# Kernel optimization log

Measured on AMD Instinct MI355X. Metric: run time of the kernel, lower is better.

Reference implementation:

```python
import jax, jax.numpy as jnp
import numpy as np

B, D = 1024, 256
Q = 65536
K = 200
CLASSES = 10
TEMP = 0.07
EPS = 1e-12  # F.normalize default eps


def _l2_normalize(v):
    n = jnp.linalg.norm(v, axis=-1, keepdims=True)
    return v / jnp.maximum(n, EPS)


def setup_inputs() -> dict:
    key = jax.random.key(0)
    k1, k2, k3 = jax.random.split(key, 3)
    x = jax.random.normal(k1, (B, D), dtype=jnp.float32)
    # memory bank init mimics uniform(-stdv, stdv) with stdv = 1/sqrt(D/3)
    stdv = 1.0 / np.sqrt(D / 3.0)
    memory = jax.random.uniform(k2, (Q, D), dtype=jnp.float32, minval=-stdv, maxval=stdv)
    memory_label = jax.random.randint(k3, (Q,), 0, CLASSES, dtype=jnp.int64)
    return {"x": x, "memory": memory, "memory_label": memory_label}


def reference(x, memory, memory_label):
    # dist: [B, Q] cosine-ish similarity (memory not re-normalized in forward)
    dist = _l2_normalize(x) @ memory.T
    # eps_ball = 1.1 > 1 -> kNN top-k branch is always taken
    sim_weight, sim_indices = jax.lax.top_k(dist, K)          # [B, K]
    sim_labels = memory_label[sim_indices]                     # [B, K]
    w = jax.nn.softmax(sim_weight / TEMP, axis=1)              # [B, K]
    one_hot = jax.nn.one_hot(sim_labels, CLASSES, dtype=w.dtype)  # [B, K, C]
    pred_scores = jnp.sum(one_hot * w[:, :, None], axis=1)     # [B, C]
    pred_scores = jnp.minimum(pred_scores + 1e-5, 1.0)
    return pred_scores
```

## Files before the change

### kernel.cpp

```cpp
#include <hip/hip_runtime.h>
#include <hip/hip_bf16.h>

#define B_ROWS 1024
#define D_DIM 256
#define Q_N 65536
#define K_TOP 200
#define N_CLASSES 10
#define INV_T 14.2857142857142857f
#define NCOLS_S 4096
#define ST_SAMP 48u
#define SCAP 4096

typedef unsigned int u32;
typedef unsigned short u16;
typedef unsigned long long u64;

using bf16x8 = __attribute__((ext_vector_type(8))) __bf16;
using f32x4  = __attribute__((ext_vector_type(4))) float;


__device__ __forceinline__ u32 fkey(float f) {
  u32 u = __float_as_uint(f);
  return (u >> 31) ? ~u : (u | 0x80000000u);
}
__device__ __forceinline__ float funkey(u32 u) {
  return __uint_as_float((u >> 31) ? (u & 0x7fffffffu) : ~u);
}
__device__ __forceinline__ u16 bf16_rn(float f) {
  u32 u = __float_as_uint(f);
  u32 r = (u + 0x7fffu + ((u >> 16) & 1u)) >> 16;
  return (u16)r;
}
__device__ __forceinline__ void split2(float f, u16& h, u16& l) {
  u16 hh = bf16_rn(f);
  float hf = __uint_as_float(((u32)hh) << 16);
  h = hh;
  l = bf16_rn(f - hf);
}

__device__ __forceinline__ void gl16(const void* g, void* l) {
  __builtin_amdgcn_global_load_lds((const __attribute__((address_space(1))) u32*)g,
                                   (__attribute__((address_space(3))) u32*)l, 16, 0, 0);
}

__global__ __launch_bounds__(256) void xnorm_k(const float* __restrict__ x,
                                               u16* __restrict__ xh, u16* __restrict__ xl) {
  int row = blockIdx.x, t = threadIdx.x;
  int lane = t & 63, w = t >> 6;
  float v = x[row * D_DIM + t];
  float s = v * v;
  for (int o = 32; o > 0; o >>= 1) s += __shfl_down(s, o);
  __shared__ float ws[4];
  if (lane == 0) ws[w] = s;
  __syncthreads();
  if (t == 0) ws[0] = ws[0] + ws[1] + ws[2] + ws[3];
  __syncthreads();
  float inv = 1.0f / fmaxf(sqrtf(ws[0]), 1e-12f);
  u16 h, l;
  split2(v * inv, h, l);
  xh[row * D_DIM + t] = h;
  xl[row * D_DIM + t] = l;
}

__global__ __launch_bounds__(256) void mdecomp_k(const float4* __restrict__ m,
                                                 ushort4* __restrict__ mh,
                                                 ushort4* __restrict__ ml, int n4) {
  int i = blockIdx.x * blockDim.x + threadIdx.x;
  int stride = gridDim.x * blockDim.x;
  for (; i < n4; i += stride) {
    float4 v = m[i];
    ushort4 h, l;
    split2(v.x, h.x, l.x);
    split2(v.y, h.y, l.y);
    split2(v.z, h.z, l.z);
    split2(v.w, h.w, l.w);
    mh[i] = h;
    ml[i] = l;
  }
}

__device__ __forceinline__ void gemm_tile(const u16* __restrict__ Ah, const u16* __restrict__ Al,
                                          const u16* __restrict__ Bh, const u16* __restrict__ Bl,
                                          int trow0, int col0, int tid, u16* sm, f32x4 (&acc)[4][4]) {
  u16* sAh = sm;
  u16* sAl = sm + 4096;
  u16* sBh = sm + 8192;
  u16* sBl = sm + 12288;
  int lane = tid & 63, wid = tid >> 6;
  int wr = wid >> 1, wc = wid & 1;

  int r_s = wid * 32 + (lane >> 2);
  int c_s = (((lane & 3) ^ ((lane >> 3) & 3)) << 3);
  int ar0 = trow0 + r_s, ar1 = ar0 + 16;
  int br0 = col0 + r_s, br1 = br0 + 16;

  int fr = lane & 15, fq = lane >> 4;
  int cswz = (fq ^ ((fr >> 1) & 3)) * 8;
  int a_off0 = (wr * 64 + fr) * 32 + cswz;
  int b_off0 = (wc * 64 + fr) * 32 + cswz;

  for (int kt = 0; kt < 8; ++kt) {
    int k0 = kt * 32;
    gl16(Ah + (size_t)ar0 * D_DIM + k0 + c_s, &sAh[wid * 1024]);
    gl16(Ah + (size_t)ar1 * D_DIM + k0 + c_s, &sAh[wid * 1024 + 512]);
    gl16(Al + (size_t)ar0 * D_DIM + k0 + c_s, &sAl[wid * 1024]);
    gl16(Al + (size_t)ar1 * D_DIM + k0 + c_s, &sAl[wid * 1024 + 512]);
    gl16(Bh + (size_t)br0 * D_DIM + k0 + c_s, &sBh[wid * 1024]);
    gl16(Bh + (size_t)br1 * D_DIM + k0 + c_s, &sBh[wid * 1024 + 512]);
    gl16(Bl + (size_t)br0 * D_DIM + k0 + c_s, &sBl[wid * 1024]);
    gl16(Bl + (size_t)br1 * D_DIM + k0 + c_s, &sBl[wid * 1024 + 512]);
    __syncthreads();

    bf16x8 ah[4], al[4], bh[4], bl[4];
#pragma unroll
    for (int m = 0; m < 4; ++m) {
      ah[m] = *(const bf16x8*)&sAh[a_off0 + m * 512];
      al[m] = *(const bf16x8*)&sAl[a_off0 + m * 512];
    }
#pragma unroll
    for (int n = 0; n < 4; ++n) {
      bh[n] = *(const bf16x8*)&sBh[b_off0 + n * 512];
      bl[n] = *(const bf16x8*)&sBl[b_off0 + n * 512];
    }
#pragma unroll
    for (int m = 0; m < 4; ++m)
#pragma unroll
      for (int n = 0; n < 4; ++n) {
        acc[m][n] = __builtin_amdgcn_mfma_f32_16x16x32_bf16(ah[m], bh[n], acc[m][n], 0, 0, 0);
        acc[m][n] = __builtin_amdgcn_mfma_f32_16x16x32_bf16(ah[m], bl[n], acc[m][n], 0, 0, 0);
        acc[m][n] = __builtin_amdgcn_mfma_f32_16x16x32_bf16(al[m], bh[n], acc[m][n], 0, 0, 0);
      }
    __syncthreads();
  }
}

__global__ __launch_bounds__(256) void gemm_s_k(const u16* __restrict__ Ah, const u16* __restrict__ Al,
                                                const u16* __restrict__ Bh, const u16* __restrict__ Bl,
                                                float* __restrict__ dist_s) {
  __shared__ u16 sm[16384];
  int tid = threadIdx.x;
  int trow0 = blockIdx.x << 7, col0 = blockIdx.y << 7;
  f32x4 acc[4][4] = {};
  gemm_tile(Ah, Al, Bh, Bl, trow0, col0, tid, sm, acc);
  int lane = tid & 63, wid = tid >> 6;
  int wr = wid >> 1, wc = wid & 1, fr = lane & 15, fq = lane >> 4;
#pragma unroll
  for (int m = 0; m < 4; ++m) {
    int rr = trow0 + wr * 64 + m * 16 + fq * 4;
#pragma unroll
    for (int n = 0; n < 4; ++n) {
      int cc = col0 + wc * 64 + n * 16 + fr;
#pragma unroll
      for (int r = 0; r < 4; ++r)
        dist_s[(size_t)(rr + r) * NCOLS_S + cc] = acc[m][n][r];
    }
  }
}

__global__ __launch_bounds__(256) void thr_k(const float* __restrict__ dist_s,
                                             u32* __restrict__ tkeyA, u32* __restrict__ cnt) {
  __shared__ u32 shist[1024];
  __shared__ u32 wtot[4];
  int row = blockIdx.x, tid = threadIdx.x, lane = tid & 63, w = tid >> 6;
  const float4* dp = (const float4*)(dist_s + (size_t)row * NCOLS_S);
  shist[tid] = 0; shist[tid + 256] = 0; shist[tid + 512] = 0; shist[tid + 768] = 0;
  __syncthreads();
#pragma unroll
  for (int j = 0; j < 4; ++j) {
    float4 v = dp[tid + (j << 8)];
    atomicAdd(&shist[fkey(v.x) >> 22], 1u);
    atomicAdd(&shist[fkey(v.y) >> 22], 1u);
    atomicAdd(&shist[fkey(v.z) >> 22], 1u);
    atomicAdd(&shist[fkey(v.w) >> 22], 1u);
  }
  __syncthreads();
  u32 cs = shist[tid * 4] + shist[tid * 4 + 1] + shist[tid * 4 + 2] + shist[tid * 4 + 3];
  u32 sfx = cs;
#pragma unroll
  for (int off = 1; off < 64; off <<= 1) {
    u32 t = __shfl_down(sfx, off);
    sfx += (lane + off < 64) ? t : 0u;
  }
  if (lane == 0) wtot[w] = sfx;
  __syncthreads();
  u32 woff = 0;
  for (int j = w + 1; j < 4; ++j) woff += wtot[j];
  u32 S = sfx + woff, Safter = S - cs;
  if (S >= ST_SAMP && Safter < ST_SAMP) {
    u32 cum = Safter;
    int bin = tid * 4;
    for (int b = tid * 4 + 3; b >= tid * 4; --b) {
      u32 hb = shist[b];
      if (cum + hb >= ST_SAMP) { bin = b; break; }
      cum += hb;
    }
    tkeyA[row] = ((u32)bin) << 22;
  }
  if (tid == 0) cnt[row] = 0;
}

__global__ __launch_bounds__(256) void gemm_f_k(const u16* __restrict__ Ah, const u16* __restrict__ Al,
                                                const u16* __restrict__ Bh, const u16* __restrict__ Bl,
                                                const u32* __restrict__ tkeyA, u32* __restrict__ cnt,
                                                u64* __restrict__ cand, int cap) {
  __shared__ u16 sm[16384];
  __shared__ u32 sT[128];
  __shared__ u32 rcnt[128], rbase[128], rcur[128];
  __shared__ u32 scnt;
  int tid = threadIdx.x;
  int bid = blockIdx.x;
  int swz = (bid & 7) * 512 + (bid >> 3);
  int trow0 = (swz & 7) << 7;
  int col0 = (swz >> 3) << 7;
  if (tid < 128) { sT[tid] = tkeyA[trow0 + tid]; rcnt[tid] = 0; }
  if (tid == 0) scnt = 0;
  f32x4 acc[4][4] = {};
  gemm_tile(Ah, Al, Bh, Bl, trow0, col0, tid, sm, acc);

  u64* sbuf = (u64*)sm;
  int lane = tid & 63, wid = tid >> 6;
  int wr = wid >> 1, wc = wid & 1, fr = lane & 15, fq = lane >> 4;
#pragma unroll
  for (int m = 0; m < 4; ++m) {
    int lr0 = wr * 64 + m * 16 + fq * 4;
#pragma unroll
    for (int n = 0; n < 4; ++n) {
      int cc = col0 + wc * 64 + n * 16 + fr;
#pragma unroll
      for (int r = 0; r < 4; ++r) {
        u32 k = fkey(acc[m][n][r]);
        int lrow = lr0 + r;
        if (k >= sT[lrow]) {
          u32 s = atomicAdd(&scnt, 1u);
          if (s < (u32)SCAP) {
            sbuf[s] = ((u64)k << 32) | ((u64)(u32)lrow << 16) | (u64)(u32)cc;
            atomicAdd(&rcnt[lrow], 1u);
          } else {
            int grow = trow0 + lrow;
            u32 s2 = atomicAdd(&cnt[grow], 1u);
            if (s2 < (u32)cap) cand[(size_t)grow * cap + s2] = ((u64)k << 32) | (u32)(~(u32)cc);
          }
        }
      }
    }
  }
  __syncthreads();
  if (tid < 128) {
    u32 nr = rcnt[tid];
    rbase[tid] = nr ? atomicAdd(&cnt[trow0 + tid], nr) : 0u;
    rcur[tid] = 0;
  }
  __syncthreads();
  u32 total = min(scnt, (u32)SCAP);
  for (u32 i = tid; i < total; i += 256) {
    u64 e = sbuf[i];
    u32 lrow = (u32)(e >> 16) & 127u;
    u32 col = (u32)e & 0xffffu;
    u32 key = (u32)(e >> 32);
    u32 off = atomicAdd(&rcur[lrow], 1u);
    u32 slot = rbase[lrow] + off;
    if (slot < (u32)cap)
      cand[(size_t)(trow0 + lrow) * cap + slot] = ((u64)key << 32) | (u32)(~col);
  }
}

__global__ __launch_bounds__(1024) void topk2_k(const u64* __restrict__ cand, const u32* __restrict__ cnt,
                                                const u32* __restrict__ tkeyA, const int* __restrict__ labels,
                                                float* __restrict__ out, int cap) {
  __shared__ u32 fhist[2048];
  __shared__ u32 wtot[16];
  __shared__ u64 bnd[2048];
  __shared__ float cls[16];
  __shared__ float den_s;
  __shared__ u32 bcnt_s, bstar_s, cab_s;
  __shared__ u64 maxp_s;
  int row = blockIdx.x, tid = threadIdx.x, lane = tid & 63, w = tid >> 6;
  u32 c = cnt[row];
  if (c > (u32)cap) c = (u32)cap;
  u32 tkey = tkeyA[row];
  const u64* cp = cand + (size_t)row * cap;

  fhist[tid] = 0; fhist[tid + 1024] = 0;
  if (tid < 16) cls[tid] = 0.f;
  if (tid == 0) { den_s = 0.f; bcnt_s = 0; bstar_s = 0; cab_s = 0; maxp_s = 0; }
  __syncthreads();

  u64 mp = 0;
  for (u32 i = tid; i < c; i += 1024) {
    u64 p = cp[i];
    mp = p > mp ? p : mp;
    u32 fb = ((u32)(p >> 32) - tkey) >> 14;
    if (fb > 2047u) fb = 2047u;
    atomicAdd(&fhist[fb], 1u);
  }
#pragma unroll
  for (int off = 32; off > 0; off >>= 1) {
    u64 t = __shfl_down(mp, off);
    mp = t > mp ? t : mp;
  }
  if (lane == 0) atomicMax((unsigned long long*)&maxp_s, (unsigned long long)mp);
  __syncthreads();
  float dmax = funkey((u32)(maxp_s >> 32));
  bool allin = (c <= K_TOP);

  if (!allin) {
    u32 cs2 = fhist[2 * tid] + fhist[2 * tid + 1];
    u32 sfx = cs2;
#pragma unroll
    for (int off = 1; off < 64; off <<= 1) {
      u32 t = __shfl_down(sfx, off);
      sfx += (lane + off < 64) ? t : 0u;
    }
    if (lane == 0) wtot[w] = sfx;
    __syncthreads();
    u32 woff = 0;
    for (int j = w + 1; j < 16; ++j) woff += wtot[j];
    u32 S = sfx + woff, Safter = S - cs2;
    if (S >= K_TOP && Safter < K_TOP) {
      u32 cum = Safter;
      int bs = 2 * tid;
      u32 cabv = 0;
      for (int b = 2 * tid + 1; b >= 2 * tid; --b) {
        u32 hb = fhist[b];
        if (cum + hb >= K_TOP) { bs = b; cabv = cum; break; }
        cum += hb;
      }
      bstar_s = (u32)bs;
      cab_s = cabv;
    }
    __syncthreads();
  }
  u32 bstar = bstar_s;
  int Kp = K_TOP - (int)cab_s;

  for (u32 i = tid; i < c; i += 1024) {
    u64 p = cp[i];
    u32 k = (u32)(p >> 32);
    u32 fb = (k - tkey) >> 14;
    if (fb > 2047u) fb = 2047u;
    if (allin || fb > bstar) {
      float wgt = __expf((funkey(k) - dmax) * INV_T);
      atomicAdd(&den_s, wgt);
      u32 col = ~(u32)(p & 0xffffffffu);
      atomicAdd(&cls[labels[col & 0xffff] & 15], wgt);
    } else if (fb == bstar) {
      u32 s2 = atomicAdd(&bcnt_s, 1u);
      if (s2 < 2048u) bnd[s2] = p;
    }
  }
  __syncthreads();
  if (!allin) {
    int bc = (int)min(bcnt_s, 2048u);
    for (int i = tid; i < bc; i += 1024) {
      u64 p = bnd[i];
      int r = 0;
      for (int j = 0; j < bc; ++j) r += (bnd[j] > p) ? 1 : 0;
      if (r < Kp) {
        u32 k = (u32)(p >> 32);
        float wgt = __expf((funkey(k) - dmax) * INV_T);
        atomicAdd(&den_s, wgt);
        u32 col = ~(u32)(p & 0xffffffffu);
        atomicAdd(&cls[labels[col & 0xffff] & 15], wgt);
      }
    }
    __syncthreads();
  }
  if (tid < N_CLASSES)
    out[(size_t)row * N_CLASSES + tid] = fminf(cls[tid] / den_s + 1e-5f, 1.0f);
}

extern "C" void kernel_launch(void* const* d_in, const int* in_sizes, int n_in,
                              void* d_out, int out_size, void* d_ws, size_t ws_size,
                              hipStream_t stream) {
  const float* x = (const float*)d_in[0];
  const float* mem = (const float*)d_in[1];
  const int* lbl = (const int*)d_in[2];
  float* out = (float*)d_out;

  char* w = (char*)d_ws;
  u16* mem_hi = (u16*)w;  w += (size_t)Q_N * D_DIM * 2;
  u16* mem_lo = (u16*)w;  w += (size_t)Q_N * D_DIM * 2;
  u16* x_hi = (u16*)w;    w += (size_t)B_ROWS * D_DIM * 2;
  u16* x_lo = (u16*)w;    w += (size_t)B_ROWS * D_DIM * 2;
  u32* tkeyA = (u32*)w;   w += (size_t)B_ROWS * 4;
  u32* cntA = (u32*)w;    w += (size_t)B_ROWS * 4;
  float* dist_s = (float*)w;  w += (size_t)B_ROWS * NCOLS_S * 4;
  u64* cand = (u64*)w;

  size_t used = (size_t)(w - (char*)d_ws);
  size_t avail = ws_size > used ? ws_size - used : 0;
  int cap = (int)(avail / ((size_t)B_ROWS * 8));
  if (cap > 12288) cap = 12288;
  if (cap < 1024) cap = 1024;

  xnorm_k<<<B_ROWS, 256, 0, stream>>>(x, x_hi, x_lo);
  mdecomp_k<<<2048, 256, 0, stream>>>((const float4*)mem, (ushort4*)mem_hi, (ushort4*)mem_lo,
                                      Q_N * D_DIM / 4);
  gemm_s_k<<<dim3(8, 32), 256, 0, stream>>>(x_hi, x_lo, mem_hi, mem_lo, dist_s);
  thr_k<<<B_ROWS, 256, 0, stream>>>(dist_s, tkeyA, cntA);
  gemm_f_k<<<4096, 256, 0, stream>>>(x_hi, x_lo, mem_hi, mem_lo, tkeyA, cntA, cand, cap);
  topk2_k<<<B_ROWS, 1024, 0, stream>>>(cand, cntA, tkeyA, lbl, out, cap);
}
```

Baseline: 314.1 us.

## Double-buffer GEMM shared-memory tiles and privatize per-wave histograms

The GEMM tile loop now uses two shared-memory buffers, so global loads for the next K-slice are issued before the MFMAs on the current slice, with one barrier per iteration instead of two. This is meant to hide global load latency behind matrix math. It doubles LDS per block (64KB), which may lower occupancy. Separately, the threshold histogram is split into per-wave private copies to cut LDS atomic contention, at the cost of more shared memory and a four-way sum during the scan.

Result: faster. 305.3 us (-2.8%).

```diff
diff --git a/kernel.cpp b/kernel.cpp
--- a/kernel.cpp
+++ b/kernel.cpp
@@ -82,10 +82,6 @@
 __device__ __forceinline__ void gemm_tile(const u16* __restrict__ Ah, const u16* __restrict__ Al,
                                           const u16* __restrict__ Bh, const u16* __restrict__ Bl,
                                           int trow0, int col0, int tid, u16* sm, f32x4 (&acc)[4][4]) {
-  u16* sAh = sm;
-  u16* sAl = sm + 4096;
-  u16* sBh = sm + 8192;
-  u16* sBl = sm + 12288;
   int lane = tid & 63, wid = tid >> 6;
   int wr = wid >> 1, wc = wid & 1;
 
@@ -99,28 +95,41 @@
   int a_off0 = (wr * 64 + fr) * 32 + cswz;
   int b_off0 = (wc * 64 + fr) * 32 + cswz;
 
+  const size_t a0 = (size_t)ar0 * D_DIM + c_s, a1 = (size_t)ar1 * D_DIM + c_s;
+  const size_t b0 = (size_t)br0 * D_DIM + c_s, b1 = (size_t)br1 * D_DIM + c_s;
+  int wbase = wid * 1024;
+
+#define STAGE(buf, kt)                                                   \
+  do {                                                                   \
+    u16* bp = sm + (buf) * 16384;                                        \
+    int k0 = (kt) * 32;                                                  \
+    gl16(Ah + a0 + k0, &bp[wbase]);                                      \
+    gl16(Ah + a1 + k0, &bp[wbase + 512]);                                \
+    gl16(Al + a0 + k0, &bp[4096 + wbase]);                               \
+    gl16(Al + a1 + k0, &bp[4096 + wbase + 512]);                         \
+    gl16(Bh + b0 + k0, &bp[8192 + wbase]);                               \
+    gl16(Bh + b1 + k0, &bp[8192 + wbase + 512]);                         \
+    gl16(Bl + b0 + k0, &bp[12288 + wbase]);                              \
+    gl16(Bl + b1 + k0, &bp[12288 + wbase + 512]);                        \
+  } while (0)
+
+  STAGE(0, 0);
+  __syncthreads();
+#pragma unroll
   for (int kt = 0; kt < 8; ++kt) {
-    int k0 = kt * 32;
-    gl16(Ah + (size_t)ar0 * D_DIM + k0 + c_s, &sAh[wid * 1024]);
-    gl16(Ah + (size_t)ar1 * D_DIM + k0 + c_s, &sAh[wid * 1024 + 512]);
-    gl16(Al + (size_t)ar0 * D_DIM + k0 + c_s, &sAl[wid * 1024]);
-    gl16(Al + (size_t)ar1 * D_DIM + k0 + c_s, &sAl[wid * 1024 + 512]);
-    gl16(Bh + (size_t)br0 * D_DIM + k0 + c_s, &sBh[wid * 1024]);
-    gl16(Bh + (size_t)br1 * D_DIM + k0 + c_s, &sBh[wid * 1024 + 512]);
-    gl16(Bl + (size_t)br0 * D_DIM + k0 + c_s, &sBl[wid * 1024]);
-    gl16(Bl + (size_t)br1 * D_DIM + k0 + c_s, &sBl[wid * 1024 + 512]);
-    __syncthreads();
-
+    int cur = kt & 1;
+    if (kt < 7) STAGE(cur ^ 1, kt + 1);
+    const u16* bp = sm + cur * 16384;
     bf16x8 ah[4], al[4], bh[4], bl[4];
 #pragma unroll
     for (int m = 0; m < 4; ++m) {
-      ah[m] = *(const bf16x8*)&sAh[a_off0 + m * 512];
-      al[m] = *(const bf16x8*)&sAl[a_off0 + m * 512];
+      ah[m] = *(const bf16x8*)&bp[a_off0 + m * 512];
+      al[m] = *(const bf16x8*)&bp[4096 + a_off0 + m * 512];
     }
 #pragma unroll
     for (int n = 0; n < 4; ++n) {
-      bh[n] = *(const bf16x8*)&sBh[b_off0 + n * 512];
-      bl[n] = *(const bf16x8*)&sBl[b_off0 + n * 512];
+      bh[n] = *(const bf16x8*)&bp[8192 + b_off0 + n * 512];
+      bl[n] = *(const bf16x8*)&bp[12288 + b_off0 + n * 512];
     }
 #pragma unroll
     for (int m = 0; m < 4; ++m)
@@ -132,12 +141,13 @@
       }
     __syncthreads();
   }
+#undef STAGE
 }
 
 __global__ __launch_bounds__(256) void gemm_s_k(const u16* __restrict__ Ah, const u16* __restrict__ Al,
                                                 const u16* __restrict__ Bh, const u16* __restrict__ Bl,
                                                 float* __restrict__ dist_s) {
-  __shared__ u16 sm[16384];
+  __shared__ u16 sm[32768];
   int tid = threadIdx.x;
   int trow0 = blockIdx.x << 7, col0 = blockIdx.y << 7;
   f32x4 acc[4][4] = {};
@@ -159,22 +169,26 @@
 
 __global__ __launch_bounds__(256) void thr_k(const float* __restrict__ dist_s,
                                              u32* __restrict__ tkeyA, u32* __restrict__ cnt) {
-  __shared__ u32 shist[1024];
+  __shared__ u32 h4[4][1024];
   __shared__ u32 wtot[4];
   int row = blockIdx.x, tid = threadIdx.x, lane = tid & 63, w = tid >> 6;
   const float4* dp = (const float4*)(dist_s + (size_t)row * NCOLS_S);
-  shist[tid] = 0; shist[tid + 256] = 0; shist[tid + 512] = 0; shist[tid + 768] = 0;
+  for (int j = tid; j < 4096; j += 256) ((u32*)h4)[j] = 0;
   __syncthreads();
 #pragma unroll
   for (int j = 0; j < 4; ++j) {
     float4 v = dp[tid + (j << 8)];
-    atomicAdd(&shist[fkey(v.x) >> 22], 1u);
-    atomicAdd(&shist[fkey(v.y) >> 22], 1u);
-    atomicAdd(&shist[fkey(v.z) >> 22], 1u);
-    atomicAdd(&shist[fkey(v.w) >> 22], 1u);
-  }
-  __syncthreads();
-  u32 cs = shist[tid * 4] + shist[tid * 4 + 1] + shist[tid * 4 + 2] + shist[tid * 4 + 3];
+    atomicAdd(&h4[w][fkey(v.x) >> 22], 1u);
+    atomicAdd(&h4[w][fkey(v.y) >> 22], 1u);
+    atomicAdd(&h4[w][fkey(v.z) >> 22], 1u);
+    atomicAdd(&h4[w][fkey(v.w) >> 22], 1u);
+  }
+  __syncthreads();
+  u32 b0 = tid * 4;
+  u32 cs = 0;
+#pragma unroll
+  for (int q = 0; q < 4; ++q)
+    cs += h4[0][b0 + q] + h4[1][b0 + q] + h4[2][b0 + q] + h4[3][b0 + q];
   u32 sfx = cs;
 #pragma unroll
   for (int off = 1; off < 64; off <<= 1) {
@@ -188,9 +202,9 @@
   u32 S = sfx + woff, Safter = S - cs;
   if (S >= ST_SAMP && Safter < ST_SAMP) {
     u32 cum = Safter;
-    int bin = tid * 4;
-    for (int b = tid * 4 + 3; b >= tid * 4; --b) {
-      u32 hb = shist[b];
+    int bin = b0;
+    for (int b = b0 + 3; b >= (int)b0; --b) {
+      u32 hb = h4[0][b] + h4[1][b] + h4[2][b] + h4[3][b];
       if (cum + hb >= ST_SAMP) { bin = b; break; }
       cum += hb;
     }
@@ -203,7 +217,7 @@
                                                 const u16* __restrict__ Bh, const u16* __restrict__ Bl,
                                                 const u32* __restrict__ tkeyA, u32* __restrict__ cnt,
                                                 u64* __restrict__ cand, int cap) {
-  __shared__ u16 sm[16384];
+  __shared__ u16 sm[32768];
   __shared__ u32 sT[128];
   __shared__ u32 rcnt[128], rbase[128], rcur[128];
   __shared__ u32 scnt;
```
